# Performance work log

Hardware: AMD Instinct MI355X
Metric: run time of the kernel (lower is better)

The kernel has to match this reference:

```python
import jax, jax.numpy as jnp
import numpy as np

ALPHA = 0.2  # LeakyReLU negative slope (module init arg)


def setup_inputs() -> dict:
    key = jax.random.key(0)
    ks = jax.random.split(key, 5)
    b, w, K, E = 8, 256, 256, 512  # batch, window_size, n_features, embed (=2*window)
    x = jax.random.normal(ks[0], (b, w, K), dtype=jnp.float32)
    W = jax.random.normal(ks[1], (E, 2 * w), dtype=jnp.float32) * 0.05
    b_lin = jax.random.normal(ks[2], (E,), dtype=jnp.float32) * 0.05
    a = jax.random.normal(ks[3], (E,), dtype=jnp.float32) * 0.05
    bias = jax.random.normal(ks[4], (K, K), dtype=jnp.float32) * 0.05
    return {"x": x, "W": W, "b_lin": b_lin, "a": a, "bias": bias}


def reference(x, W, b_lin, a, bias):
    # x: (b, window, K) -> v: (b, K, window)
    v = jnp.transpose(x, (0, 2, 1))
    w = v.shape[2]
    # lin(concat(v_i, v_j)) == v_i @ Wl^T + v_j @ Wr^T + b_lin  (split weight)
    Wl, Wr = W[:, :w], W[:, w:]
    left = jnp.einsum('bkw,ew->bke', v, Wl)    # (b, K, E)
    right = jnp.einsum('bkw,ew->bke', v, Wr)   # (b, K, E)
    pre = left[:, :, None, :] + right[:, None, :, :] + b_lin  # (b, K, K, E)
    act = jax.nn.leaky_relu(pre, negative_slope=ALPHA)
    e = jnp.einsum('bije,e->bij', act, a) + bias               # (b, K, K)
    attn = jax.nn.softmax(e, axis=2)  # dropout p=0 in eval -> identity
    h = jax.nn.sigmoid(jnp.einsum('bij,bjw->biw', attn, v))    # (b, K, window)
    return jnp.transpose(h, (0, 2, 1))                          # (b, window, K)
```

## Files before the change

kernel.cpp:

```cpp
#include <hip/hip_runtime.h>
#include <math.h>

typedef float f32x4 __attribute__((ext_vector_type(4)));
typedef __bf16 bf16x8 __attribute__((ext_vector_type(8)));
typedef unsigned short u16x8 __attribute__((ext_vector_type(8)));

__device__ __forceinline__ unsigned short f2bf(float f) {
    union { float f; unsigned int u; } v; v.f = f;
    unsigned int u = v.u;
    return (unsigned short)((u + 0x7fffu + ((u >> 16) & 1u)) >> 16);
}
__device__ __forceinline__ float bf_lo(unsigned int d) {
    union { unsigned int u; float f; } v; v.u = d << 16; return v.f;
}
__device__ __forceinline__ float bf_hi(unsigned int d) {
    union { unsigned int u; float f; } v; v.u = d & 0xffff0000u; return v.f;
}
__device__ __forceinline__ float sigmoidf_(float v) {
    return 1.f / (1.f + __expf(-v));
}

__global__ __launch_bounds__(256) void mfma_gemm_kernel(
    const float* __restrict__ x,
    const float* __restrict__ W,
    const float* __restrict__ b_lin,
    float* __restrict__ LpT,
    unsigned short* __restrict__ R2,
    unsigned short* __restrict__ xbf)
{
    const int b = blockIdx.y;
    const int t = blockIdx.x;

    if (t >= 64) {
        const int idx = b * 65536 + (t - 64) * 2048 + threadIdx.x * 8;
        const float4 v0 = *(const float4*)(x + idx);
        const float4 v1 = *(const float4*)(x + idx + 4);
        u16x8 o;
        o[0] = f2bf(v0.x); o[1] = f2bf(v0.y); o[2] = f2bf(v0.z); o[3] = f2bf(v0.w);
        o[4] = f2bf(v1.x); o[5] = f2bf(v1.y); o[6] = f2bf(v1.z); o[7] = f2bf(v1.w);
        *(u16x8*)(xbf + idx) = o;
        return;
    }

    const bool left = (t < 32);
    int m0, n0;
    if (left) { m0 = (t >> 3) * 64; n0 = (t & 7) * 64; }
    else      { const int tt = t - 32; m0 = (tt >> 2) * 64; n0 = (tt & 3) * 64; }

    __shared__ unsigned short As[64][72];
    __shared__ unsigned short Bs[64][72];

    unsigned short (*Ts)[72] = left ? As : Bs;
    unsigned short (*Ds)[72] = left ? Bs : As;
    const int cbase = left ? m0 : n0;
    const int rbase = left ? n0 : m0;
    const int coff  = left ? 0 : 256;

    const int tid  = threadIdx.x;
    const int wv   = tid >> 6;
    const int lane = tid & 63;
    const int wy = wv >> 1, wx = wv & 1;
    const int lr = lane & 15;
    const int lk = lane >> 4;

    const float* xb = x + b * 65536;

    f32x4 acc[2][2];
    #pragma unroll
    for (int i = 0; i < 2; i++)
        #pragma unroll
        for (int jj = 0; jj < 2; jj++) acc[i][jj] = (f32x4){0.f, 0.f, 0.f, 0.f};

    const int wl = tid >> 4;
    const int kg = tid & 15;
    const int dr = tid >> 2;
    const int dc = (tid & 3) * 16;

    for (int k0 = 0; k0 < 256; k0 += 64) {
        #pragma unroll
        for (int p = 0; p < 4; p++) {
            const int w = wl + 16 * p;
            const float4 v = *(const float4*)(xb + (k0 + w) * 256 + cbase + kg * 4);
            Ts[kg * 4 + 0][w] = f2bf(v.x);
            Ts[kg * 4 + 1][w] = f2bf(v.y);
            Ts[kg * 4 + 2][w] = f2bf(v.z);
            Ts[kg * 4 + 3][w] = f2bf(v.w);
        }
        {
            const float* src = W + (rbase + dr) * 512 + coff + k0 + dc;
            const float4 v0 = *(const float4*)(src);
            const float4 v1 = *(const float4*)(src + 4);
            const float4 v2 = *(const float4*)(src + 8);
            const float4 v3 = *(const float4*)(src + 12);
            u16x8 o0, o1;
            o0[0] = f2bf(v0.x); o0[1] = f2bf(v0.y); o0[2] = f2bf(v0.z); o0[3] = f2bf(v0.w);
            o0[4] = f2bf(v1.x); o0[5] = f2bf(v1.y); o0[6] = f2bf(v1.z); o0[7] = f2bf(v1.w);
            o1[0] = f2bf(v2.x); o1[1] = f2bf(v2.y); o1[2] = f2bf(v2.z); o1[3] = f2bf(v2.w);
            o1[4] = f2bf(v3.x); o1[5] = f2bf(v3.y); o1[6] = f2bf(v3.z); o1[7] = f2bf(v3.w);
            *(u16x8*)&Ds[dr][dc]     = o0;
            *(u16x8*)&Ds[dr][dc + 8] = o1;
        }
        __syncthreads();
        #pragma unroll
        for (int kk = 0; kk < 64; kk += 32) {
            const bf16x8 a0 = *(const bf16x8*)&As[wy * 32 + lr][kk + lk * 8];
            const bf16x8 a1 = *(const bf16x8*)&As[wy * 32 + 16 + lr][kk + lk * 8];
            const bf16x8 b0 = *(const bf16x8*)&Bs[wx * 32 + lr][kk + lk * 8];
            const bf16x8 b1 = *(const bf16x8*)&Bs[wx * 32 + 16 + lr][kk + lk * 8];
            acc[0][0] = __builtin_amdgcn_mfma_f32_16x16x32_bf16(a0, b0, acc[0][0], 0, 0, 0);
            acc[0][1] = __builtin_amdgcn_mfma_f32_16x16x32_bf16(a0, b1, acc[0][1], 0, 0, 0);
            acc[1][0] = __builtin_amdgcn_mfma_f32_16x16x32_bf16(a1, b0, acc[1][0], 0, 0, 0);
            acc[1][1] = __builtin_amdgcn_mfma_f32_16x16x32_bf16(a1, b1, acc[1][1], 0, 0, 0);
        }
        __syncthreads();
    }

    if (left) {
        #pragma unroll
        for (int mi = 0; mi < 2; mi++) {
            #pragma unroll
            for (int ni = 0; ni < 2; ni++) {
                const int row = m0 + wy * 32 + mi * 16 + lk * 4;
                const int col = n0 + wx * 32 + ni * 16 + lr;
                const float bl = b_lin[col];
                float4 o;
                o.x = acc[mi][ni][0] + bl;
                o.y = acc[mi][ni][1] + bl;
                o.z = acc[mi][ni][2] + bl;
                o.w = acc[mi][ni][3] + bl;
                *(float4*)(LpT + b * 131072 + (row >> 2) * 2048 + col * 4) = o;
            }
        }
    } else {
        unsigned short* R2b = R2 + b * 131072;
        #pragma unroll
        for (int mi = 0; mi < 2; mi++) {
            #pragma unroll
            for (int ni = 0; ni < 2; ni++) {
                const int row = m0 + wy * 32 + mi * 16 + lk * 4;
                const int col = n0 + wx * 32 + ni * 16 + lr;
                ushort4 o;
                o.x = f2bf(acc[mi][ni][0]);
                o.y = f2bf(acc[mi][ni][1]);
                o.z = f2bf(acc[mi][ni][2]);
                o.w = f2bf(acc[mi][ni][3]);
                *(ushort4*)(R2b + (row >> 3) * 2048 + col * 8 + (row & 7)) = o;
            }
        }
    }
}

__global__ __launch_bounds__(1024, 8) void attn_kernel(
    const unsigned short* __restrict__ xbf,
    const float* __restrict__ LpT,
    const unsigned int* __restrict__ R2u,
    const float* __restrict__ a,
    const float* __restrict__ bias,
    float* __restrict__ out)
{
    const int b     = blockIdx.x & 7;
    const int itile = blockIdx.x >> 3;
    const int i0    = itile * 4;
    const int tid   = threadIdx.x;
    const int j     = tid & 255;
    const int wv    = tid >> 6;
    const int lane  = tid & 63;

    __shared__ float acc2P[4][4][256];
    __shared__ float rgp[4][256];
    __shared__ float u15p[8][4];
    __shared__ unsigned short atbf[16 * 264];

    const int ehq = __builtin_amdgcn_readfirstlane(tid >> 8);

    const float* Lq = LpT + b * 131072 + itile * 2048 + ehq * 512;
    const float* aq = a + ehq * 128;
    const uint4* Rq = (const uint4*)(R2u + b * 65536) + (ehq * 16) * 256 + j;

    uint4 rb0 = Rq[0];
    uint4 rb1 = Rq[256];

    if (tid < 512) {
        const float4 lv = *(const float4*)(LpT + b * 131072 + itile * 2048 + tid * 4);
        const float ae = a[tid];
        float p0 = ae * lv.x, p1 = ae * lv.y, p2 = ae * lv.z, p3 = ae * lv.w;
        #pragma unroll
        for (int off = 32; off; off >>= 1) {
            p0 += __shfl_xor(p0, off);
            p1 += __shfl_xor(p1, off);
            p2 += __shfl_xor(p2, off);
            p3 += __shfl_xor(p3, off);
        }
        if (lane == 0) {
            u15p[wv][0] = p0; u15p[wv][1] = p1;
            u15p[wv][2] = p2; u15p[wv][3] = p3;
        }
    }

    float acc0 = 0.f, acc1 = 0.f, acc2 = 0.f, acc3 = 0.f, rsum = 0.f;

    #pragma unroll 2
    for (int tk = 0; tk < 16; tk++) {
        uint4 rb2;
        if (tk < 14) rb2 = Rq[(tk + 2) * 256];
        float r[8];
        r[0] = bf_lo(rb0.x); r[1] = bf_hi(rb0.x);
        r[2] = bf_lo(rb0.y); r[3] = bf_hi(rb0.y);
        r[4] = bf_lo(rb0.z); r[5] = bf_hi(rb0.z);
        r[6] = bf_lo(rb0.w); r[7] = bf_hi(rb0.w);
        #pragma unroll
        for (int g = 0; g < 2; g++) {
            const float4 av4 = *(const float4*)(aq + tk * 8 + g * 4);
            const float4 l0 = *(const float4*)(Lq + (tk * 8 + g * 4 + 0) * 4);
            const float4 l1 = *(const float4*)(Lq + (tk * 8 + g * 4 + 1) * 4);
            const float4 l2 = *(const float4*)(Lq + (tk * 8 + g * 4 + 2) * 4);
            const float4 l3 = *(const float4*)(Lq + (tk * 8 + g * 4 + 3) * 4);
            const float rv0 = r[g * 4 + 0];
            const float rv1 = r[g * 4 + 1];
            const float rv2 = r[g * 4 + 2];
            const float rv3 = r[g * 4 + 3];
            rsum = fmaf(av4.x, rv0, rsum);
            acc0 = fmaf(av4.x, fabsf(l0.x + rv0), acc0);
            acc1 = fmaf(av4.x, fabsf(l0.y + rv0), acc1);
            acc2 = fmaf(av4.x, fabsf(l0.z + rv0), acc2);
            acc3 = fmaf(av4.x, fabsf(l0.w + rv0), acc3);
            rsum = fmaf(av4.y, rv1, rsum);
            acc0 = fmaf(av4.y, fabsf(l1.x + rv1), acc0);
            acc1 = fmaf(av4.y, fabsf(l1.y + rv1), acc1);
            acc2 = fmaf(av4.y, fabsf(l1.z + rv1), acc2);
            acc3 = fmaf(av4.y, fabsf(l1.w + rv1), acc3);
            rsum = fmaf(av4.z, rv2, rsum);
            acc0 = fmaf(av4.z, fabsf(l2.x + rv2), acc0);
            acc1 = fmaf(av4.z, fabsf(l2.y + rv2), acc1);
            acc2 = fmaf(av4.z, fabsf(l2.z + rv2), acc2);
            acc3 = fmaf(av4.z, fabsf(l2.w + rv2), acc3);
            rsum = fmaf(av4.w, rv3, rsum);
            acc0 = fmaf(av4.w, fabsf(l3.x + rv3), acc0);
            acc1 = fmaf(av4.w, fabsf(l3.y + rv3), acc1);
            acc2 = fmaf(av4.w, fabsf(l3.z + rv3), acc2);
            acc3 = fmaf(av4.w, fabsf(l3.w + rv3), acc3);
        }
        rb0 = rb1;
        rb1 = rb2;
    }
    acc2P[ehq][0][j] = acc0;
    acc2P[ehq][1][j] = acc1;
    acc2P[ehq][2][j] = acc2;
    acc2P[ehq][3][j] = acc3;
    rgp[ehq][j] = rsum;
    __syncthreads();

    if (wv < 4) {
        const int i = wv;
        float u15 = 0.f;
        #pragma unroll
        for (int q = 0; q < 8; q++) u15 += u15p[q][i];
        u15 *= 0.6f;
        float v[4];
        float m = -1e30f;
        #pragma unroll
        for (int u = 0; u < 4; u++) {
            const int jj = lane + 64 * u;
            const float uR = rgp[0][jj] + rgp[1][jj] + rgp[2][jj] + rgp[3][jj];
            const float ab = acc2P[0][i][jj] + acc2P[1][i][jj]
                           + acc2P[2][i][jj] + acc2P[3][i][jj];
            v[u] = u15 + 0.6f * uR + 0.4f * ab + bias[(i0 + i) * 256 + jj];
            m = fmaxf(m, v[u]);
        }
        #pragma unroll
        for (int off = 32; off; off >>= 1) m = fmaxf(m, __shfl_xor(m, off));
        float ssum = 0.f;
        #pragma unroll
        for (int u = 0; u < 4; u++) { v[u] = __expf(v[u] - m); ssum += v[u]; }
        #pragma unroll
        for (int off = 32; off; off >>= 1) ssum += __shfl_xor(ssum, off);
        const float inv = 1.f / ssum;
        #pragma unroll
        for (int u = 0; u < 4; u++)
            atbf[i * 264 + lane + 64 * u] = f2bf(v[u] * inv);
    }
    __syncthreads();

    {
        const int lr = lane & 15;
        const int lk = lane >> 4;
        f32x4 hacc = (f32x4){0.f, 0.f, 0.f, 0.f};
        const unsigned short* xw = xbf + b * 65536 + (wv * 16 + lr) * 256;
        #pragma unroll
        for (int kt = 0; kt < 8; kt++) {
            const bf16x8 av = *(const bf16x8*)&atbf[lr * 264 + kt * 32 + lk * 8];
            const bf16x8 bv = *(const bf16x8*)(xw + kt * 32 + lk * 8);
            hacc = __builtin_amdgcn_mfma_f32_16x16x32_bf16(av, bv, hacc, 0, 0, 0);
        }
        if (lk == 0) {
            float4 o;
            o.x = sigmoidf_(hacc[0]);
            o.y = sigmoidf_(hacc[1]);
            o.z = sigmoidf_(hacc[2]);
            o.w = sigmoidf_(hacc[3]);
            *(float4*)(out + b * 65536 + (wv * 16 + lr) * 256 + i0) = o;
        }
    }
}

extern "C" void kernel_launch(void* const* d_in, const int* in_sizes, int n_in,
                              void* d_out, int out_size, void* d_ws, size_t ws_size,
                              hipStream_t stream) {
    const float* x     = (const float*)d_in[0];
    const float* W     = (const float*)d_in[1];
    const float* b_lin = (const float*)d_in[2];
    const float* a     = (const float*)d_in[3];
    const float* bias  = (const float*)d_in[4];
    float* out = (float*)d_out;

    char* ws = (char*)d_ws;
    float*          LpT = (float*)ws;
    unsigned short* R2  = (unsigned short*)(ws + (4 << 20));
    unsigned short* xbf = (unsigned short*)(ws + (6 << 20));

    mfma_gemm_kernel<<<dim3(96, 8), 256, 0, stream>>>(x, W, b_lin, LpT, R2, xbf);
    attn_kernel<<<512, 1024, 0, stream>>>(xbf, LpT, (const unsigned int*)R2, a, bias, out);
}
```

Before: 102.2 us.

## Store right projection in fp32 and prefetch GEMM tiles into registers

The right-half projection R is now written and read as fp32 instead of packed bf16. This removes the bf16 unpack work in the attention inner loop and the extra rounding error, but doubles the bytes the attention kernel loads per j. The GEMM kernel now loads the next K-tile of x and W into registers before the barrier, overlapping global loads with the MFMA work. f2bf uses the native __bf16 conversion, the attention loop unroll goes from 2 to 4, and the workspace layout is shifted to fit the larger buffer.

```diff
diff --git a/kernel.cpp b/kernel.cpp
--- a/kernel.cpp
+++ b/kernel.cpp
@@ -6,15 +6,10 @@
 typedef unsigned short u16x8 __attribute__((ext_vector_type(8)));
 
 __device__ __forceinline__ unsigned short f2bf(float f) {
-    union { float f; unsigned int u; } v; v.f = f;
-    unsigned int u = v.u;
-    return (unsigned short)((u + 0x7fffu + ((u >> 16) & 1u)) >> 16);
-}
-__device__ __forceinline__ float bf_lo(unsigned int d) {
-    union { unsigned int u; float f; } v; v.u = d << 16; return v.f;
-}
-__device__ __forceinline__ float bf_hi(unsigned int d) {
-    union { unsigned int u; float f; } v; v.u = d & 0xffff0000u; return v.f;
+    __bf16 h = (__bf16)f;
+    unsigned short u;
+    __builtin_memcpy(&u, &h, 2);
+    return u;
 }
 __device__ __forceinline__ float sigmoidf_(float v) {
     return 1.f / (1.f + __expf(-v));
@@ -25,7 +20,7 @@
     const float* __restrict__ W,
     const float* __restrict__ b_lin,
     float* __restrict__ LpT,
-    unsigned short* __restrict__ R2,
+    float* __restrict__ R2f,
     unsigned short* __restrict__ xbf)
 {
     const int b = blockIdx.y;
@@ -76,29 +71,48 @@
     const int dr = tid >> 2;
     const int dc = (tid & 3) * 16;
 
+    float4 xr0, xr1, xr2, xr3, wq0, wq1, wq2, wq3;
+    {
+        xr0 = *(const float4*)(xb + (wl +  0) * 256 + cbase + kg * 4);
+        xr1 = *(const float4*)(xb + (wl + 16) * 256 + cbase + kg * 4);
+        xr2 = *(const float4*)(xb + (wl + 32) * 256 + cbase + kg * 4);
+        xr3 = *(const float4*)(xb + (wl + 48) * 256 + cbase + kg * 4);
+        const float* src = W + (rbase + dr) * 512 + coff + dc;
+        wq0 = *(const float4*)(src);
+        wq1 = *(const float4*)(src + 4);
+        wq2 = *(const float4*)(src + 8);
+        wq3 = *(const float4*)(src + 12);
+    }
+
     for (int k0 = 0; k0 < 256; k0 += 64) {
-        #pragma unroll
-        for (int p = 0; p < 4; p++) {
-            const int w = wl + 16 * p;
-            const float4 v = *(const float4*)(xb + (k0 + w) * 256 + cbase + kg * 4);
-            Ts[kg * 4 + 0][w] = f2bf(v.x);
-            Ts[kg * 4 + 1][w] = f2bf(v.y);
-            Ts[kg * 4 + 2][w] = f2bf(v.z);
-            Ts[kg * 4 + 3][w] = f2bf(v.w);
-        }
+        Ts[kg*4+0][wl+ 0]=f2bf(xr0.x); Ts[kg*4+1][wl+ 0]=f2bf(xr0.y);
+        Ts[kg*4+2][wl+ 0]=f2bf(xr0.z); Ts[kg*4+3][wl+ 0]=f2bf(xr0.w);
+        Ts[kg*4+0][wl+16]=f2bf(xr1.x); Ts[kg*4+1][wl+16]=f2bf(xr1.y);
+        Ts[kg*4+2][wl+16]=f2bf(xr1.z); Ts[kg*4+3][wl+16]=f2bf(xr1.w);
+        Ts[kg*4+0][wl+32]=f2bf(xr2.x); Ts[kg*4+1][wl+32]=f2bf(xr2.y);
+        Ts[kg*4+2][wl+32]=f2bf(xr2.z); Ts[kg*4+3][wl+32]=f2bf(xr2.w);
+        Ts[kg*4+0][wl+48]=f2bf(xr3.x); Ts[kg*4+1][wl+48]=f2bf(xr3.y);
+        Ts[kg*4+2][wl+48]=f2bf(xr3.z); Ts[kg*4+3][wl+48]=f2bf(xr3.w);
         {
-            const float* src = W + (rbase + dr) * 512 + coff + k0 + dc;
-            const float4 v0 = *(const float4*)(src);
-            const float4 v1 = *(const float4*)(src + 4);
-            const float4 v2 = *(const float4*)(src + 8);
-            const float4 v3 = *(const float4*)(src + 12);
             u16x8 o0, o1;
-            o0[0] = f2bf(v0.x); o0[1] = f2bf(v0.y); o0[2] = f2bf(v0.z); o0[3] = f2bf(v0.w);
-            o0[4] = f2bf(v1.x); o0[5] = f2bf(v1.y); o0[6] = f2bf(v1.z); o0[7] = f2bf(v1.w);
-            o1[0] = f2bf(v2.x); o1[1] = f2bf(v2.y); o1[2] = f2bf(v2.z); o1[3] = f2bf(v2.w);
-            o1[4] = f2bf(v3.x); o1[5] = f2bf(v3.y); o1[6] = f2bf(v3.z); o1[7] = f2bf(v3.w);
+            o0[0]=f2bf(wq0.x); o0[1]=f2bf(wq0.y); o0[2]=f2bf(wq0.z); o0[3]=f2bf(wq0.w);
+            o0[4]=f2bf(wq1.x); o0[5]=f2bf(wq1.y); o0[6]=f2bf(wq1.z); o0[7]=f2bf(wq1.w);
+            o1[0]=f2bf(wq2.x); o1[1]=f2bf(wq2.y); o1[2]=f2bf(wq2.z); o1[3]=f2bf(wq2.w);
+            o1[4]=f2bf(wq3.x); o1[5]=f2bf(wq3.y); o1[6]=f2bf(wq3.z); o1[7]=f2bf(wq3.w);
             *(u16x8*)&Ds[dr][dc]     = o0;
             *(u16x8*)&Ds[dr][dc + 8] = o1;
+        }
+        if (k0 < 192) {
+            const int kn = k0 + 64;
+            xr0 = *(const float4*)(xb + (kn + wl +  0) * 256 + cbase + kg * 4);
+            xr1 = *(const float4*)(xb + (kn + wl + 16) * 256 + cbase + kg * 4);
+            xr2 = *(const float4*)(xb + (kn + wl + 32) * 256 + cbase + kg * 4);
+            xr3 = *(const float4*)(xb + (kn + wl + 48) * 256 + cbase + kg * 4);
+            const float* src = W + (rbase + dr) * 512 + coff + kn + dc;
+            wq0 = *(const float4*)(src);
+            wq1 = *(const float4*)(src + 4);
+            wq2 = *(const float4*)(src + 8);
+            wq3 = *(const float4*)(src + 12);
         }
         __syncthreads();
         #pragma unroll
@@ -132,19 +146,19 @@
             }
         }
     } else {
-        unsigned short* R2b = R2 + b * 131072;
+        float* R2b = R2f + b * 131072;
         #pragma unroll
         for (int mi = 0; mi < 2; mi++) {
             #pragma unroll
             for (int ni = 0; ni < 2; ni++) {
                 const int row = m0 + wy * 32 + mi * 16 + lk * 4;
                 const int col = n0 + wx * 32 + ni * 16 + lr;
-                ushort4 o;
-                o.x = f2bf(acc[mi][ni][0]);
-                o.y = f2bf(acc[mi][ni][1]);
-                o.z = f2bf(acc[mi][ni][2]);
-                o.w = f2bf(acc[mi][ni][3]);
-                *(ushort4*)(R2b + (row >> 3) * 2048 + col * 8 + (row & 7)) = o;
+                float4 o;
+                o.x = acc[mi][ni][0];
+                o.y = acc[mi][ni][1];
+                o.z = acc[mi][ni][2];
+                o.w = acc[mi][ni][3];
+                *(float4*)(R2b + (row >> 3) * 2048 + col * 8 + (row & 7)) = o;
             }
         }
     }
@@ -153,7 +167,7 @@
 __global__ __launch_bounds__(1024, 8) void attn_kernel(
     const unsigned short* __restrict__ xbf,
     const float* __restrict__ LpT,
-    const unsigned int* __restrict__ R2u,
+    const float* __restrict__ R2f,
     const float* __restrict__ a,
     const float* __restrict__ bias,
     float* __restrict__ out)
@@ -175,10 +189,10 @@
 
     const float* Lq = LpT + b * 131072 + itile * 2048 + ehq * 512;
     const float* aq = a + ehq * 128;
-    const uint4* Rq = (const uint4*)(R2u + b * 65536) + (ehq * 16) * 256 + j;
-
-    uint4 rb0 = Rq[0];
-    uint4 rb1 = Rq[256];
+    const float4* Rp = (const float4*)(R2f + b * 131072 + (ehq * 16) * 2048) + j * 2;
+
+    float4 cA0 = Rp[0],   cA1 = Rp[1];
+    float4 cB0 = Rp[512], cB1 = Rp[513];
 
     if (tid < 512) {
         const float4 lv = *(const float4*)(LpT + b * 131072 + itile * 2048 + tid * 4);
@@ -199,15 +213,10 @@
 
     float acc0 = 0.f, acc1 = 0.f, acc2 = 0.f, acc3 = 0.f, rsum = 0.f;
 
-    #pragma unroll 2
+    #pragma unroll 4
     for (int tk = 0; tk < 16; tk++) {
-        uint4 rb2;
-        if (tk < 14) rb2 = Rq[(tk + 2) * 256];
-        float r[8];
-        r[0] = bf_lo(rb0.x); r[1] = bf_hi(rb0.x);
-        r[2] = bf_lo(rb0.y); r[3] = bf_hi(rb0.y);
-        r[4] = bf_lo(rb0.z); r[5] = bf_hi(rb0.z);
-        r[6] = bf_lo(rb0.w); r[7] = bf_hi(rb0.w);
+        float4 cC0, cC1;
+        if (tk < 14) { cC0 = Rp[(tk + 2) * 512]; cC1 = Rp[(tk + 2) * 512 + 1]; }
         #pragma unroll
         for (int g = 0; g < 2; g++) {
             const float4 av4 = *(const float4*)(aq + tk * 8 + g * 4);
@@ -215,10 +224,10 @@
             const float4 l1 = *(const float4*)(Lq + (tk * 8 + g * 4 + 1) * 4);
             const float4 l2 = *(const float4*)(Lq + (tk * 8 + g * 4 + 2) * 4);
             const float4 l3 = *(const float4*)(Lq + (tk * 8 + g * 4 + 3) * 4);
-            const float rv0 = r[g * 4 + 0];
-            const float rv1 = r[g * 4 + 1];
-            const float rv2 = r[g * 4 + 2];
-            const float rv3 = r[g * 4 + 3];
+            const float rv0 = g ? cA1.x : cA0.x;
+            const float rv1 = g ? cA1.y : cA0.y;
+            const float rv2 = g ? cA1.z : cA0.z;
+            const float rv3 = g ? cA1.w : cA0.w;
             rsum = fmaf(av4.x, rv0, rsum);
             acc0 = fmaf(av4.x, fabsf(l0.x + rv0), acc0);
             acc1 = fmaf(av4.x, fabsf(l0.y + rv0), acc1);
@@ -240,8 +249,8 @@
             acc2 = fmaf(av4.w, fabsf(l3.z + rv3), acc2);
             acc3 = fmaf(av4.w, fabsf(l3.w + rv3), acc3);
         }
-        rb0 = rb1;
-        rb1 = rb2;
+        cA0 = cB0; cA1 = cB1;
+        cB0 = cC0; cB1 = cC1;
     }
     acc2P[ehq][0][j] = acc0;
     acc2P[ehq][1][j] = acc1;
@@ -315,9 +324,9 @@
 
     char* ws = (char*)d_ws;
     float*          LpT = (float*)ws;
-    unsigned short* R2  = (unsigned short*)(ws + (4 << 20));
-    unsigned short* xbf = (unsigned short*)(ws + (6 << 20));
-
-    mfma_gemm_kernel<<<dim3(96, 8), 256, 0, stream>>>(x, W, b_lin, LpT, R2, xbf);
-    attn_kernel<<<512, 1024, 0, stream>>>(xbf, LpT, (const unsigned int*)R2, a, bias, out);
-}
+    float*          R2f = (float*)(ws + (4 << 20));
+    unsigned short* xbf = (unsigned short*)(ws + (8 << 20));
+
+    mfma_gemm_kernel<<<dim3(96, 8), 256, 0, stream>>>(x, W, b_lin, LpT, R2f, xbf);
+    attn_kernel<<<512, 1024, 0, stream>>>(xbf, LpT, R2f, a, bias, out);
+}
```

New measurement: 110.3 us. 7.9% more time.

## Halve attention block to 2 rows and 512 threads, prefetch x for output GEMM

Applied to the files above, without the earlier changes.

The attention kernel now handles 2 query rows per block with 512 threads split into 2 embedding halves, instead of 4 rows with 1024 threads split into 4 quarters. The grid doubles to 1024 blocks. Each wave now computes two 16-column output tiles. Part of the bf16 x operand is preloaded before the softmax barrier so its global latency overlaps the softmax. This targets better occupancy and load balance, at the cost of reading R twice as often per query row and doing less work per block.

```diff
diff --git a/kernel.cpp b/kernel.cpp
--- a/kernel.cpp
+++ b/kernel.cpp
@@ -93,10 +93,10 @@
             const float4 v2 = *(const float4*)(src + 8);
             const float4 v3 = *(const float4*)(src + 12);
             u16x8 o0, o1;
-            o0[0] = f2bf(v0.x); o0[1] = f2bf(v0.y); o0[2] = f2bf(v0.z); o0[3] = f2bf(v0.w);
-            o0[4] = f2bf(v1.x); o0[5] = f2bf(v1.y); o0[6] = f2bf(v1.z); o0[7] = f2bf(v1.w);
-            o1[0] = f2bf(v2.x); o1[1] = f2bf(v2.y); o1[2] = f2bf(v2.z); o1[3] = f2bf(v2.w);
-            o1[4] = f2bf(v3.x); o1[5] = f2bf(v3.y); o1[6] = f2bf(v3.z); o1[7] = f2bf(v3.w);
+            o0[0]=f2bf(v0.x); o0[1]=f2bf(v0.y); o0[2]=f2bf(v0.z); o0[3]=f2bf(v0.w);
+            o0[4]=f2bf(v1.x); o0[5]=f2bf(v1.y); o0[6]=f2bf(v1.z); o0[7]=f2bf(v1.w);
+            o1[0]=f2bf(v2.x); o1[1]=f2bf(v2.y); o1[2]=f2bf(v2.z); o1[3]=f2bf(v2.w);
+            o1[4]=f2bf(v3.x); o1[5]=f2bf(v3.y); o1[6]=f2bf(v3.z); o1[7]=f2bf(v3.w);
             *(u16x8*)&Ds[dr][dc]     = o0;
             *(u16x8*)&Ds[dr][dc + 8] = o1;
         }
@@ -150,7 +150,7 @@
     }
 }
 
-__global__ __launch_bounds__(1024, 8) void attn_kernel(
+__global__ __launch_bounds__(512, 8) void attn_kernel(
     const unsigned short* __restrict__ xbf,
     const float* __restrict__ LpT,
     const unsigned int* __restrict__ R2u,
@@ -158,51 +158,49 @@
     const float* __restrict__ bias,
     float* __restrict__ out)
 {
-    const int b     = blockIdx.x & 7;
-    const int itile = blockIdx.x >> 3;
-    const int i0    = itile * 4;
-    const int tid   = threadIdx.x;
-    const int j     = tid & 255;
-    const int wv    = tid >> 6;
-    const int lane  = tid & 63;
-
-    __shared__ float acc2P[4][4][256];
-    __shared__ float rgp[4][256];
-    __shared__ float u15p[8][4];
+    const int blk  = (int)blockIdx.x;
+    const int b    = blk & 7;
+    const int it2  = blk >> 3;
+    const int i0   = it2 * 2;
+    const int tid  = threadIdx.x;
+    const int j    = tid & 255;
+    const int wv   = tid >> 6;
+    const int lane = tid & 63;
+
+    __shared__ float acc2P[2][2][256];
+    __shared__ float rgp[2][256];
+    __shared__ float u15p[8][2];
     __shared__ unsigned short atbf[16 * 264];
 
-    const int ehq = __builtin_amdgcn_readfirstlane(tid >> 8);
-
-    const float* Lq = LpT + b * 131072 + itile * 2048 + ehq * 512;
-    const float* aq = a + ehq * 128;
-    const uint4* Rq = (const uint4*)(R2u + b * 65536) + (ehq * 16) * 256 + j;
+    const int eh = __builtin_amdgcn_readfirstlane(tid >> 8);
+
+    const float* Lq = LpT + b * 131072 + (it2 >> 1) * 2048 + (it2 & 1) * 2
+                    + eh * 256 * 4;
+    const float* aq = a + eh * 256;
+    const uint4* Rq = (const uint4*)(R2u + b * 65536) + (eh * 32) * 256 + j;
 
     uint4 rb0 = Rq[0];
     uint4 rb1 = Rq[256];
 
-    if (tid < 512) {
-        const float4 lv = *(const float4*)(LpT + b * 131072 + itile * 2048 + tid * 4);
+    {
+        const float2 lv = *(const float2*)(LpT + b * 131072 + (it2 >> 1) * 2048
+                                           + tid * 4 + (it2 & 1) * 2);
         const float ae = a[tid];
-        float p0 = ae * lv.x, p1 = ae * lv.y, p2 = ae * lv.z, p3 = ae * lv.w;
+        float p0 = ae * lv.x, p1 = ae * lv.y;
         #pragma unroll
         for (int off = 32; off; off >>= 1) {
             p0 += __shfl_xor(p0, off);
             p1 += __shfl_xor(p1, off);
-            p2 += __shfl_xor(p2, off);
-            p3 += __shfl_xor(p3, off);
-        }
-        if (lane == 0) {
-            u15p[wv][0] = p0; u15p[wv][1] = p1;
-            u15p[wv][2] = p2; u15p[wv][3] = p3;
-        }
-    }
-
-    float acc0 = 0.f, acc1 = 0.f, acc2 = 0.f, acc3 = 0.f, rsum = 0.f;
+        }
+        if (lane == 0) { u15p[wv][0] = p0; u15p[wv][1] = p1; }
+    }
+
+    float acc0 = 0.f, acc1 = 0.f, rsum = 0.f;
 
     #pragma unroll 2
-    for (int tk = 0; tk < 16; tk++) {
+    for (int tk = 0; tk < 32; tk++) {
         uint4 rb2;
-        if (tk < 14) rb2 = Rq[(tk + 2) * 256];
+        if (tk < 30) rb2 = Rq[(tk + 2) * 256];
         float r[8];
         r[0] = bf_lo(rb0.x); r[1] = bf_hi(rb0.x);
         r[2] = bf_lo(rb0.y); r[3] = bf_hi(rb0.y);
@@ -211,10 +209,10 @@
         #pragma unroll
         for (int g = 0; g < 2; g++) {
             const float4 av4 = *(const float4*)(aq + tk * 8 + g * 4);
-            const float4 l0 = *(const float4*)(Lq + (tk * 8 + g * 4 + 0) * 4);
-            const float4 l1 = *(const float4*)(Lq + (tk * 8 + g * 4 + 1) * 4);
-            const float4 l2 = *(const float4*)(Lq + (tk * 8 + g * 4 + 2) * 4);
-            const float4 l3 = *(const float4*)(Lq + (tk * 8 + g * 4 + 3) * 4);
+            const float2 l0 = *(const float2*)(Lq + (tk * 8 + g * 4 + 0) * 4);
+            const float2 l1 = *(const float2*)(Lq + (tk * 8 + g * 4 + 1) * 4);
+            const float2 l2 = *(const float2*)(Lq + (tk * 8 + g * 4 + 2) * 4);
+            const float2 l3 = *(const float2*)(Lq + (tk * 8 + g * 4 + 3) * 4);
             const float rv0 = r[g * 4 + 0];
             const float rv1 = r[g * 4 + 1];
             const float rv2 = r[g * 4 + 2];
@@ -222,35 +220,33 @@
             rsum = fmaf(av4.x, rv0, rsum);
             acc0 = fmaf(av4.x, fabsf(l0.x + rv0), acc0);
             acc1 = fmaf(av4.x, fabsf(l0.y + rv0), acc1);
-            acc2 = fmaf(av4.x, fabsf(l0.z + rv0), acc2);
-            acc3 = fmaf(av4.x, fabsf(l0.w + rv0), acc3);
             rsum = fmaf(av4.y, rv1, rsum);
             acc0 = fmaf(av4.y, fabsf(l1.x + rv1), acc0);
             acc1 = fmaf(av4.y, fabsf(l1.y + rv1), acc1);
-            acc2 = fmaf(av4.y, fabsf(l1.z + rv1), acc2);
-            acc3 = fmaf(av4.y, fabsf(l1.w + rv1), acc3);
             rsum = fmaf(av4.z, rv2, rsum);
             acc0 = fmaf(av4.z, fabsf(l2.x + rv2), acc0);
             acc1 = fmaf(av4.z, fabsf(l2.y + rv2), acc1);
-            acc2 = fmaf(av4.z, fabsf(l2.z + rv2), acc2);
-            acc3 = fmaf(av4.z, fabsf(l2.w + rv2), acc3);
             rsum = fmaf(av4.w, rv3, rsum);
             acc0 = fmaf(av4.w, fabsf(l3.x + rv3), acc0);
             acc1 = fmaf(av4.w, fabsf(l3.y + rv3), acc1);
-            acc2 = fmaf(av4.w, fabsf(l3.z + rv3), acc2);
-            acc3 = fmaf(av4.w, fabsf(l3.w + rv3), acc3);
         }
         rb0 = rb1;
         rb1 = rb2;
     }
-    acc2P[ehq][0][j] = acc0;
-    acc2P[ehq][1][j] = acc1;
-    acc2P[ehq][2][j] = acc2;
-    acc2P[ehq][3][j] = acc3;
-    rgp[ehq][j] = rsum;
+    acc2P[eh][0][j] = acc0;
+    acc2P[eh][1][j] = acc1;
+    rgp[eh][j] = rsum;
     __syncthreads();
 
-    if (wv < 4) {
+    const int lr = lane & 15;
+    const int lk = lane >> 4;
+    const unsigned short* xw0 = xbf + b * 65536 + (wv * 16 + lr) * 256;
+    const bf16x8 px0 = *(const bf16x8*)(xw0 + 0 * 32 + lk * 8);
+    const bf16x8 px1 = *(const bf16x8*)(xw0 + 1 * 32 + lk * 8);
+    const bf16x8 px2 = *(const bf16x8*)(xw0 + 2 * 32 + lk * 8);
+    const bf16x8 px3 = *(const bf16x8*)(xw0 + 3 * 32 + lk * 8);
+
+    if (wv < 2) {
         const int i = wv;
         float u15 = 0.f;
         #pragma unroll
@@ -261,9 +257,8 @@
         #pragma unroll
         for (int u = 0; u < 4; u++) {
             const int jj = lane + 64 * u;
-            const float uR = rgp[0][jj] + rgp[1][jj] + rgp[2][jj] + rgp[3][jj];
-            const float ab = acc2P[0][i][jj] + acc2P[1][i][jj]
-                           + acc2P[2][i][jj] + acc2P[3][i][jj];
+            const float uR = rgp[0][jj] + rgp[1][jj];
+            const float ab = acc2P[0][i][jj] + acc2P[1][i][jj];
             v[u] = u15 + 0.6f * uR + 0.4f * ab + bias[(i0 + i) * 256 + jj];
             m = fmaxf(m, v[u]);
         }
@@ -282,23 +277,43 @@
     __syncthreads();
 
     {
-        const int lr = lane & 15;
-        const int lk = lane >> 4;
         f32x4 hacc = (f32x4){0.f, 0.f, 0.f, 0.f};
-        const unsigned short* xw = xbf + b * 65536 + (wv * 16 + lr) * 256;
+        {
+            const bf16x8 a0 = *(const bf16x8*)&atbf[lr * 264 + 0 * 32 + lk * 8];
+            hacc = __builtin_amdgcn_mfma_f32_16x16x32_bf16(a0, px0, hacc, 0, 0, 0);
+            const bf16x8 a1 = *(const bf16x8*)&atbf[lr * 264 + 1 * 32 + lk * 8];
+            hacc = __builtin_amdgcn_mfma_f32_16x16x32_bf16(a1, px1, hacc, 0, 0, 0);
+            const bf16x8 a2 = *(const bf16x8*)&atbf[lr * 264 + 2 * 32 + lk * 8];
+            hacc = __builtin_amdgcn_mfma_f32_16x16x32_bf16(a2, px2, hacc, 0, 0, 0);
+            const bf16x8 a3 = *(const bf16x8*)&atbf[lr * 264 + 3 * 32 + lk * 8];
+            hacc = __builtin_amdgcn_mfma_f32_16x16x32_bf16(a3, px3, hacc, 0, 0, 0);
+            #pragma unroll
+            for (int kt = 4; kt < 8; kt++) {
+                const bf16x8 av = *(const bf16x8*)&atbf[lr * 264 + kt * 32 + lk * 8];
+                const bf16x8 bv = *(const bf16x8*)(xw0 + kt * 32 + lk * 8);
+                hacc = __builtin_amdgcn_mfma_f32_16x16x32_bf16(av, bv, hacc, 0, 0, 0);
+            }
+        }
+        if (lk == 0) {
+            float2 o;
+            o.x = sigmoidf_(hacc[0]);
+            o.y = sigmoidf_(hacc[1]);
+            *(float2*)(out + b * 65536 + (wv * 16 + lr) * 256 + i0) = o;
+        }
+        const int nt = wv + 8;
+        f32x4 hacc2 = (f32x4){0.f, 0.f, 0.f, 0.f};
+        const unsigned short* xw = xbf + b * 65536 + (nt * 16 + lr) * 256;
         #pragma unroll
         for (int kt = 0; kt < 8; kt++) {
             const bf16x8 av = *(const bf16x8*)&atbf[lr * 264 + kt * 32 + lk * 8];
             const bf16x8 bv = *(const bf16x8*)(xw + kt * 32 + lk * 8);
-            hacc = __builtin_amdgcn_mfma_f32_16x16x32_bf16(av, bv, hacc, 0, 0, 0);
+            hacc2 = __builtin_amdgcn_mfma_f32_16x16x32_bf16(av, bv, hacc2, 0, 0, 0);
         }
         if (lk == 0) {
-            float4 o;
-            o.x = sigmoidf_(hacc[0]);
-            o.y = sigmoidf_(hacc[1]);
-            o.z = sigmoidf_(hacc[2]);
-            o.w = sigmoidf_(hacc[3]);
-            *(float4*)(out + b * 65536 + (wv * 16 + lr) * 256 + i0) = o;
+            float2 o;
+            o.x = sigmoidf_(hacc2[0]);
+            o.y = sigmoidf_(hacc2[1]);
+            *(float2*)(out + b * 65536 + (nt * 16 + lr) * 256 + i0) = o;
         }
     }
 }
@@ -319,5 +334,6 @@
     unsigned short* xbf = (unsigned short*)(ws + (6 << 20));
 
     mfma_gemm_kernel<<<dim3(96, 8), 256, 0, stream>>>(x, W, b_lin, LpT, R2, xbf);
-    attn_kernel<<<512, 1024, 0, stream>>>(xbf, LpT, (const unsigned int*)R2, a, bias, out);
-}
+    attn_kernel<<<1024, 512, 0, stream>>>(xbf, LpT, (const unsigned int*)R2,
+                                          a, bias, out);
+}
```

After: 109.8 us. 1.07x slower.
